# Kernel optimization log

Measured on AMD Instinct MI355X. Metric: run time of the kernel, lower is better.

The kernel has to match this reference:

```python
import jax, jax.numpy as jnp
import numpy as np

B, S, D = 2, 2048, 4096
NH, NKV = 32, 8
HD = D // NH          # 128
NREP = NH // NKV      # 4 (GQA groups)


def _rope(t, cos, sin):
    # t: [b, s, h, d]; cos/sin: [s, d//2]; interleaved (real, imag) pairs on last dim
    tr = t.reshape(*t.shape[:-1], -1, 2)
    a, b = tr[..., 0], tr[..., 1]
    c = cos[None, :, None, :]
    s = sin[None, :, None, :]
    out = jnp.stack([a * c - b * s, a * s + b * c], axis=-1)
    return out.reshape(t.shape)


def _repeat_kv(t, n_rep):
    # [b, s, n_kv, d] -> [b, s, n_kv*n_rep, d]
    b, s, nkv, d = t.shape
    return jnp.broadcast_to(t[:, :, :, None, :], (b, s, nkv, n_rep, d)).reshape(b, s, nkv * n_rep, d)


def setup_inputs() -> dict:
    key = jax.random.key(0)
    ks = jax.random.split(key, 5)
    x = jax.random.normal(ks[0], (B, S, D), jnp.float32)
    wq = jax.random.normal(ks[1], (D, NH * HD), jnp.float32) * 0.02
    wk = jax.random.normal(ks[2], (D, NKV * HD), jnp.float32) * 0.02
    wv = jax.random.normal(ks[3], (D, NKV * HD), jnp.float32) * 0.02
    wo = jax.random.normal(ks[4], (NH * HD, D), jnp.float32) * 0.02
    inv_freq = 1.0 / (10000.0 ** (jnp.arange(0, HD, 2, dtype=jnp.float32) / HD))
    angles = jnp.arange(S, dtype=jnp.float32)[:, None] * inv_freq[None, :]  # [S, HD//2]
    return {
        "x": x, "wq": wq, "wk": wk, "wv": wv, "wo": wo,
        "freqs_cos": jnp.cos(angles), "freqs_sin": jnp.sin(angles),
        "start_pos": 0,
    }


def reference(x, wq, wk, wv, wo, freqs_cos, freqs_sin, start_pos):
    b, s, _ = x.shape
    xq = (x @ wq).reshape(b, s, NH, HD)
    xk = (x @ wk).reshape(b, s, NKV, HD)
    xv = (x @ wv).reshape(b, s, NKV, HD)
    xq = _rope(xq, freqs_cos, freqs_sin)
    xk = _rope(xk, freqs_cos, freqs_sin)
    # prefill (start_pos=0): cache[:b, :s] = xk/xv, then keys/values read back equal xk/xv
    keys = _repeat_kv(xk, NREP)    # [b, s, NH, HD]
    values = _repeat_kv(xv, NREP)  # [b, s, NH, HD]
    scores = jnp.einsum("bqhd,bkhd->bhqk", xq, keys) / jnp.sqrt(jnp.float32(HD))
    probs = jax.nn.softmax(scores, axis=-1)
    out = jnp.einsum("bhqk,bkhd->bqhd", probs, values).reshape(b, s, NH * HD)
    return out @ wo
```

## Files before the change

### kernel.cpp

```cpp
#include <hip/hip_runtime.h>
#include <hip/hip_bf16.h>
#include <cstdint>

#define B_   2
#define S_   2048
#define D_   4096
#define NH_  32
#define NKV_ 8
#define HD_  128
#define BS_  (B_*S_)
#define NQK_ 6144

typedef __bf16 bf16_t;
typedef __bf16 bf16x8 __attribute__((ext_vector_type(8)));
typedef __bf16 bf16x4 __attribute__((ext_vector_type(4)));
typedef __bf16 bf16x2 __attribute__((ext_vector_type(2)));
typedef float  f32x4  __attribute__((ext_vector_type(4)));

typedef const __attribute__((address_space(1))) void* gas_ptr;
typedef __attribute__((address_space(3))) void* las_ptr;

__device__ __forceinline__ void gload_lds16(const void* g, void* l) {
  __builtin_amdgcn_global_load_lds((gas_ptr)g, (las_ptr)l, 16, 0, 0);
}

__device__ __forceinline__ float exp2_fast(float x) {
  float r;
  asm("v_exp_f32 %0, %1" : "=v"(r) : "v"(x));
  return r;
}

#define LD8(p) (*(const bf16x8*)(p))
#define MFMA(a, b, c) __builtin_amdgcn_mfma_f32_16x16x32_bf16(a, b, c, 0, 0, 0)

__global__ __launch_bounds__(256) void k_cvt(const float4* __restrict__ in,
                                             bf16x4* __restrict__ out, int n4) {
  int i = blockIdx.x * 256 + threadIdx.x;
  if (i >= n4) return;
  float4 v = in[i];
  bf16x4 o = { (bf16_t)v.x, (bf16_t)v.y, (bf16_t)v.z, (bf16_t)v.w };
  out[i] = o;
}

__global__ __launch_bounds__(256) void k_transpose_cvt(const float* __restrict__ w,
                                                       bf16_t* __restrict__ wt,
                                                       int K, int N) {
  __shared__ float tile[32][33];
  int n0 = blockIdx.x * 32, k0 = blockIdx.y * 32;
  int tx = threadIdx.x, ty = threadIdx.y;
#pragma unroll
  for (int i = 0; i < 4; i++)
    tile[ty + 8*i][tx] = w[(size_t)(k0 + ty + 8*i) * N + n0 + tx];
  __syncthreads();
#pragma unroll
  for (int i = 0; i < 4; i++)
    wt[(size_t)(n0 + ty + 8*i) * K + k0 + tx] = (bf16_t)tile[tx][ty + 8*i];
}

template <typename CT, int NF>
__global__ __launch_bounds__(512, 2) void k_gemm8p(const bf16_t* __restrict__ A,
                                                   const bf16_t* __restrict__ Bt,
                                                   CT* __restrict__ C,
                                                   int M, int N, int K) {
  __shared__ __align__(16) bf16_t As[2][256 * 64];
  __shared__ __align__(16) bf16_t Bs[2][NF * 64 * 64];
  const int tid = threadIdx.x;
  const int l = tid & 63, w = tid >> 6;
  const int lr = l & 15, lg = l >> 4;
  const int wm = w >> 2, wn = w & 3;

  const int bm = blockIdx.x, bn = blockIdx.y;

  const bf16_t* Ab = A  + (size_t)bm * 256 * K;
  const bf16_t* Bb = Bt + (size_t)bn * (NF * 64) * K;

  int st_row[4], st_col[4], st_dst[4];
#pragma unroll
  for (int j = 0; j < 4; j++) {
    int o = (j * 512 + tid) * 16;
    int row = o >> 7, cb = o & 127;
    st_row[j] = row;
    st_col[j] = (cb ^ ((row & 7) << 4)) >> 1;
    st_dst[j] = o >> 1;
  }

  int aoff[8], boff[NF];
#pragma unroll
  for (int m = 0; m < 8; m++) {
    int r = wm * 128 + m * 16 + lr;
    aoff[m] = r * 64 + (((lg * 16) ^ ((r & 7) << 4)) >> 1);
  }
#pragma unroll
  for (int n = 0; n < NF; n++) {
    int r = wn * (16 * NF) + n * 16 + lr;
    boff[n] = r * 64 + (((lg * 16) ^ ((r & 7) << 4)) >> 1);
  }

  f32x4 acc[8][NF];
#pragma unroll
  for (int m = 0; m < 8; m++)
#pragma unroll
    for (int n = 0; n < NF; n++) acc[m][n] = f32x4{0.f, 0.f, 0.f, 0.f};

  auto stageA = [&](int k, int h) {
    const int kt = k << 6;
    const int rof = h << 7;
#pragma unroll
    for (int j = 0; j < 2; j++)
      gload_lds16(Ab + (size_t)(st_row[j] + rof) * K + kt + st_col[j],
                  &As[k & 1][0] + (rof << 6) + st_dst[j]);
  };
  auto stageB = [&](int k) {
    const int kt = k << 6;
#pragma unroll
    for (int j = 0; j < NF; j++)
      gload_lds16(Bb + (size_t)st_row[j] * K + kt + st_col[j],
                  &Bs[k & 1][0] + st_dst[j]);
  };

  const int NT = K >> 6;
  stageA(0, 0); stageA(0, 1); stageB(0); stageB(1);
  if constexpr (NF == 3) asm volatile("s_waitcnt vmcnt(3)" ::: "memory");
  else                   asm volatile("s_waitcnt vmcnt(4)" ::: "memory");
  __builtin_amdgcn_s_barrier();

  for (int k = 0; k < NT; ++k) {
    const bf16_t* Ap = &As[k & 1][0];
    const bf16_t* Bp = &Bs[k & 1][0];
    const bool s1 = (k + 1 < NT), s2 = (k + 2 < NT);
    bf16x8 bfr[NF], a[4];

#pragma unroll
    for (int n = 0; n < NF; n++) bfr[n] = LD8(Bp + boff[n]);
#pragma unroll
    for (int m = 0; m < 4; m++) a[m] = LD8(Ap + aoff[m]);
    if (s1) stageA(k + 1, 0);
    __builtin_amdgcn_s_barrier();
    asm volatile("s_waitcnt lgkmcnt(0)" ::: "memory");
    __builtin_amdgcn_s_setprio(1);
#pragma unroll
    for (int m = 0; m < 4; m++)
#pragma unroll
      for (int n = 0; n < NF; n++)
        acc[m][n] = MFMA(a[m], bfr[n], acc[m][n]);
    __builtin_amdgcn_s_setprio(0);
    __builtin_amdgcn_s_barrier();

#pragma unroll
    for (int m = 0; m < 4; m++) a[m] = LD8(Ap + aoff[m + 4]);
    if (s1) stageA(k + 1, 1);
    __builtin_amdgcn_s_barrier();
    asm volatile("s_waitcnt lgkmcnt(0)" ::: "memory");
    __builtin_amdgcn_s_setprio(1);
#pragma unroll
    for (int m = 0; m < 4; m++)
#pragma unroll
      for (int n = 0; n < NF; n++)
        acc[m + 4][n] = MFMA(a[m], bfr[n], acc[m + 4][n]);
    __builtin_amdgcn_s_setprio(0);
    __builtin_amdgcn_s_barrier();

#pragma unroll
    for (int n = 0; n < NF; n++) bfr[n] = LD8(Bp + (boff[n] ^ 32));
#pragma unroll
    for (int m = 0; m < 4; m++) a[m] = LD8(Ap + (aoff[m] ^ 32));
    __builtin_amdgcn_s_barrier();
    asm volatile("s_waitcnt lgkmcnt(0)" ::: "memory");
    __builtin_amdgcn_s_setprio(1);
#pragma unroll
    for (int m = 0; m < 4; m++)
#pragma unroll
      for (int n = 0; n < NF; n++)
        acc[m][n] = MFMA(a[m], bfr[n], acc[m][n]);
    __builtin_amdgcn_s_setprio(0);
    __builtin_amdgcn_s_barrier();

#pragma unroll
    for (int m = 0; m < 4; m++) a[m] = LD8(Ap + (aoff[m + 4] ^ 32));
    if (s2) {
      stageB(k + 2);
      if constexpr (NF == 3) asm volatile("s_waitcnt vmcnt(3)" ::: "memory");
      else                   asm volatile("s_waitcnt vmcnt(4)" ::: "memory");
    } else if (s1) {
      asm volatile("s_waitcnt vmcnt(0)" ::: "memory");
    }
    __builtin_amdgcn_s_barrier();
    asm volatile("s_waitcnt lgkmcnt(0)" ::: "memory");
    __builtin_amdgcn_s_setprio(1);
#pragma unroll
    for (int m = 0; m < 4; m++)
#pragma unroll
      for (int n = 0; n < NF; n++)
        acc[m + 4][n] = MFMA(a[m], bfr[n], acc[m + 4][n]);
    __builtin_amdgcn_s_setprio(0);
    __builtin_amdgcn_s_barrier();
  }

#pragma unroll
  for (int m = 0; m < 8; m++) {
    int row0 = bm * 256 + wm * 128 + m * 16 + lg * 4;
#pragma unroll
    for (int n = 0; n < NF; n++) {
      int col = bn * (NF * 64) + wn * (16 * NF) + n * 16 + lr;
#pragma unroll
      for (int i = 0; i < 4; i++)
        C[(size_t)(row0 + i) * N + col] = (CT)acc[m][n][i];
    }
  }
}

__global__ __launch_bounds__(256) void k_rope(const bf16_t* __restrict__ qkv,
                                              const float* __restrict__ fcos,
                                              const float* __restrict__ fsin,
                                              bf16_t* __restrict__ dst,
                                              int nheads, int col_off, float mul) {
  int idx = blockIdx.x * 256 + threadIdx.x;
  int p = idx & 63;
  int h = (idx >> 6) % nheads;
  int bs = idx / (64 * nheads);
  int s = bs & (S_ - 1);
  int b = bs >> 11;
  const bf16_t* src = qkv + (size_t)bs * NQK_ + col_off + h * HD_ + 2 * p;
  bf16x2 ab = *(const bf16x2*)src;
  float a = (float)ab[0], bb = (float)ab[1];
  float c = fcos[s * 64 + p], sn = fsin[s * 64 + p];
  bf16x2 o = { (bf16_t)((a * c - bb * sn) * mul), (bf16_t)((a * sn + bb * c) * mul) };
  *(bf16x2*)(dst + ((((size_t)b * nheads + h) * S_ + s) * HD_) + 2 * p) = o;
}

__global__ __launch_bounds__(256) void k_vtrans(const bf16_t* __restrict__ qkv,
                                                bf16_t* __restrict__ vtr) {
  __shared__ bf16_t tile[32][33];
  int s0 = blockIdx.x * 32, d0 = blockIdx.y * 32, z = blockIdx.z;
  int b = z >> 3, kvh = z & 7;
  int tx = threadIdx.x, ty = threadIdx.y;
#pragma unroll
  for (int i = 0; i < 4; i++)
    tile[ty + 8*i][tx] =
        qkv[(size_t)(b * S_ + s0 + ty + 8*i) * NQK_ + (D_ + NKV_ * HD_) + kvh * HD_ + d0 + tx];
  __syncthreads();
#pragma unroll
  for (int i = 0; i < 4; i++)
    vtr[((size_t)z * HD_ + d0 + ty + 8*i) * S_ + s0 + tx] = tile[tx][ty + 8*i];
}

#define KVBLK 64
#define SM_THR 12.0f
__global__ __launch_bounds__(256, 2) void k_flash(const bf16_t* __restrict__ qr,
                                                  const bf16_t* __restrict__ kr,
                                                  const bf16_t* __restrict__ vt,
                                                  bf16_t* __restrict__ ctx) {
  __shared__ __align__(16) bf16_t Ks[2][KVBLK * HD_];
  __shared__ __align__(16) bf16_t Vs[2][HD_ * KVBLK];
  __shared__ __align__(16) char  plds[4][2048];
  const int tid = threadIdx.x;
  const int l = tid & 63, w = tid >> 6;
  const int lr = l & 15, lg = l >> 4;
  const int qb = blockIdx.x, h = blockIdx.y, b = blockIdx.z;
  const int kvh = h >> 2;

  const bf16_t* qbase = qr + (((size_t)b * NH_ + h) * S_ + qb * 128 + w * 32) * HD_;
  const bf16_t* kbase = kr + (((size_t)b * NKV_ + kvh) * S_) * HD_;
  const bf16_t* vbase = vt + (((size_t)b * NKV_ + kvh) * HD_) * S_;

  bf16x8 qf[2][4];
#pragma unroll
  for (int m = 0; m < 2; m++)
#pragma unroll
    for (int kk = 0; kk < 4; kk++)
      qf[m][kk] = *(const bf16x8*)(qbase + (m * 16 + lr) * HD_ + kk * 32 + lg * 8);

  bf16x8 ones;
#pragma unroll
  for (int j = 0; j < 8; j++) ones[j] = (bf16_t)1.0f;

  f32x4 o[2][9];
#pragma unroll
  for (int m = 0; m < 2; m++)
#pragma unroll
    for (int n = 0; n < 9; n++) o[m][n] = f32x4{0.f, 0.f, 0.f, 0.f};
  float mR[2][4];
#pragma unroll
  for (int m = 0; m < 2; m++)
#pragma unroll
    for (int i = 0; i < 4; i++) mR[m][i] = -1e30f;

  auto stage = [&](int bu, int t) {
    const int kb = t * KVBLK;
#pragma unroll
    for (int j = 0; j < 4; j++) {
      int o_ = (tid + 256 * j) * 16;
      int row = o_ >> 8, cb = o_ & 255;
      int scb = cb ^ ((row & 7) << 4);
      gload_lds16(kbase + (size_t)(kb + row) * HD_ + (scb >> 1),
                  &Ks[bu][0] + (o_ >> 1));
    }
#pragma unroll
    for (int j = 0; j < 4; j++) {
      int o_ = (tid + 256 * j) * 16;
      int row = o_ >> 7, cb = o_ & 127;
      int scb = cb ^ ((row & 7) << 4);
      gload_lds16(vbase + (size_t)row * S_ + kb + (scb >> 1),
                  &Vs[bu][0] + (o_ >> 1));
    }
  };

  const int nt = S_ / KVBLK;
  stage(0, 0);
  __syncthreads();
  int buf = 0;

  for (int t = 0; t < nt; t++) {
    if (t + 1 < nt) stage(buf ^ 1, t + 1);
    const bf16_t* Kb = &Ks[buf][0];
    const bf16_t* Vb = &Vs[buf][0];

    f32x4 sc[2][4];
#pragma unroll
    for (int m = 0; m < 2; m++)
#pragma unroll
      for (int n = 0; n < 4; n++) sc[m][n] = f32x4{0.f, 0.f, 0.f, 0.f};
    __builtin_amdgcn_s_setprio(1);
#pragma unroll
    for (int n = 0; n < 4; n++) {
#pragma unroll
      for (int kk = 0; kk < 4; kk++) {
        int r = n * 16 + lr;
        int cb = (kk * 64 + lg * 16) ^ ((r & 7) << 4);
        bf16x8 kf = *(const bf16x8*)(Kb + (((r << 8) + cb) >> 1));
        sc[0][n] = MFMA(qf[0][kk], kf, sc[0][n]);
        sc[1][n] = MFMA(qf[1][kk], kf, sc[1][n]);
      }
    }
    __builtin_amdgcn_s_setprio(0);

    bf16x8 pf[2][2];
#pragma unroll
    for (int m = 0; m < 2; m++) {
      float chk = -1e30f;
#pragma unroll
      for (int i = 0; i < 4; i++) {
        float lm = fmaxf(fmaxf(sc[m][0][i], sc[m][1][i]),
                         fmaxf(sc[m][2][i], sc[m][3][i]));
        chk = fmaxf(chk, lm - mR[m][i]);
      }
      if (!__all(chk <= SM_THR)) {
#pragma unroll
        for (int i = 0; i < 4; i++) {
          float tmx = fmaxf(fmaxf(sc[m][0][i], sc[m][1][i]),
                            fmaxf(sc[m][2][i], sc[m][3][i]));
          tmx = fmaxf(tmx, __shfl_xor(tmx, 1));
          tmx = fmaxf(tmx, __shfl_xor(tmx, 2));
          tmx = fmaxf(tmx, __shfl_xor(tmx, 4));
          tmx = fmaxf(tmx, __shfl_xor(tmx, 8));
          float mnew = fmaxf(mR[m][i], tmx);
          float alpha = exp2_fast(mR[m][i] - mnew);
          mR[m][i] = mnew;
#pragma unroll
          for (int n = 0; n < 9; n++) o[m][n][i] *= alpha;
        }
      }
#pragma unroll
      for (int n = 0; n < 4; n++)
#pragma unroll
        for (int i = 0; i < 4; i++) {
          float pv = exp2_fast(sc[m][n][i] - mR[m][i]);
          int r = lg * 4 + i;
          int cbyte = (n * 32 + lr * 2) ^ ((r & 7) << 4);
          *(bf16_t*)(&plds[w][r * 128 + cbyte]) = (bf16_t)pv;
        }
      pf[m][0] = *(const bf16x8*)(&plds[w][lr * 128 + ((lg * 16) ^ ((lr & 7) << 4))]);
      pf[m][1] = *(const bf16x8*)(&plds[w][lr * 128 + ((64 + lg * 16) ^ ((lr & 7) << 4))]);
    }

    __builtin_amdgcn_s_setprio(1);
#pragma unroll
    for (int n = 0; n < 8; n++) {
#pragma unroll
      for (int kk = 0; kk < 2; kk++) {
        int r = n * 16 + lr;
        int cb = (kk * 64 + lg * 16) ^ ((r & 7) << 4);
        bf16x8 vf = *(const bf16x8*)(Vb + (((r << 7) + cb) >> 1));
        o[0][n] = MFMA(pf[0][kk], vf, o[0][n]);
        o[1][n] = MFMA(pf[1][kk], vf, o[1][n]);
      }
    }
    o[0][8] = MFMA(pf[0][0], ones, o[0][8]);
    o[0][8] = MFMA(pf[0][1], ones, o[0][8]);
    o[1][8] = MFMA(pf[1][0], ones, o[1][8]);
    o[1][8] = MFMA(pf[1][1], ones, o[1][8]);
    __builtin_amdgcn_s_setprio(0);
    __syncthreads();
    buf ^= 1;
  }

#pragma unroll
  for (int m = 0; m < 2; m++)
#pragma unroll
    for (int i = 0; i < 4; i++) {
      float inv = 1.0f / o[m][8][i];
      int srow = qb * 128 + w * 32 + m * 16 + lg * 4 + i;
#pragma unroll
      for (int n = 0; n < 8; n++) {
        int d = n * 16 + lr;
        ctx[((size_t)(b * S_ + srow)) * D_ + h * HD_ + d] = (bf16_t)(o[m][n][i] * inv);
      }
    }
}

extern "C" void kernel_launch(void* const* d_in, const int* in_sizes, int n_in,
                              void* d_out, int out_size, void* d_ws, size_t ws_size,
                              hipStream_t stream) {
  const float* x    = (const float*)d_in[0];
  const float* wq   = (const float*)d_in[1];
  const float* wk   = (const float*)d_in[2];
  const float* wv   = (const float*)d_in[3];
  const float* wo   = (const float*)d_in[4];
  const float* fcos = (const float*)d_in[5];
  const float* fsin = (const float*)d_in[6];
  float* out = (float*)d_out;

  const size_t SZ_XB    = (size_t)BS_ * D_ * 2;
  const size_t SZ_WQKVT = (size_t)NQK_ * D_ * 2;
  const size_t SZ_WOT   = (size_t)D_ * D_ * 2;
  char* p = (char*)d_ws;
  bf16_t* xb    = (bf16_t*)p;
  bf16_t* wqkvt = (bf16_t*)(p + SZ_XB);
  bf16_t* wot   = (bf16_t*)(p + SZ_XB + SZ_WQKVT);
  bf16_t* qkv   = (bf16_t*)(p + SZ_XB + SZ_WQKVT + SZ_WOT);
  bf16_t* qrope = xb;
  bf16_t* krope = wqkvt;
  bf16_t* vtr   = wqkvt + (size_t)BS_ * NKV_ * HD_;
  bf16_t* ctx   = qkv;

  const float QSCALE = (float)(0.08838834764831845 * 1.4426950408889634);

  dim3 tb(32, 8);
  k_cvt<<<BS_ * D_ / 1024, 256, 0, stream>>>((const float4*)x, (bf16x4*)xb, BS_ * D_ / 4);
  k_transpose_cvt<<<dim3(D_ / 32, D_ / 32), tb, 0, stream>>>(wq, wqkvt, D_, D_);
  k_transpose_cvt<<<dim3(32, D_ / 32), tb, 0, stream>>>(wk, wqkvt + (size_t)D_ * D_, D_, NKV_ * HD_);
  k_transpose_cvt<<<dim3(32, D_ / 32), tb, 0, stream>>>(wv, wqkvt + (size_t)(D_ + NKV_ * HD_) * D_, D_, NKV_ * HD_);
  k_transpose_cvt<<<dim3(D_ / 32, D_ / 32), tb, 0, stream>>>(wo, wot, D_, D_);
  k_gemm8p<bf16_t, 3><<<dim3(BS_ / 256, NQK_ / 192), 512, 0, stream>>>(xb, wqkvt, qkv, BS_, NQK_, D_);
  k_rope<<<BS_ * NH_ * 64 / 256, 256, 0, stream>>>(qkv, fcos, fsin, qrope, NH_, 0, QSCALE);
  k_rope<<<BS_ * NKV_ * 64 / 256, 256, 0, stream>>>(qkv, fcos, fsin, krope, NKV_, D_, 1.0f);
  k_vtrans<<<dim3(S_ / 32, HD_ / 32, B_ * NKV_), tb, 0, stream>>>(qkv, vtr);
  k_flash<<<dim3(S_ / 128, NH_, B_), 256, 0, stream>>>(qrope, krope, vtr, ctx);
  k_gemm8p<float, 4><<<dim3(BS_ / 256, D_ / 256), 512, 0, stream>>>(ctx, wot, out, BS_, D_, D_);
}
```

Measured before the change: 606.7 us.

## Transpose QK^T MFMA operands and shuffle P through registers instead of LDS

Swaps the A/B operands of the score MFMA so each lane holds one query row's scores. The row max then comes from an in-lane reduction plus two cross-lane shuffles, and each lane keeps a single running max per row. The P tile is now packed with v_cvt_pk_bf16 and rearranged into the PV operand layout with ds_bpermute, replacing the per-element LDS stores and reloads and their scratch buffer. This removes LDS traffic and shuffle work from the softmax step but adds bpermute operations and a per-row alpha broadcast. The remaining 60 lines of the kernel, which finalize with mR, are not shown and may need matching changes.

```diff
diff --git a/kernel.cpp b/kernel.cpp
--- a/kernel.cpp
+++ b/kernel.cpp
@@ -16,6 +16,7 @@
 typedef __bf16 bf16x4 __attribute__((ext_vector_type(4)));
 typedef __bf16 bf16x2 __attribute__((ext_vector_type(2)));
 typedef float  f32x4  __attribute__((ext_vector_type(4)));
+typedef unsigned uint32x4 __attribute__((ext_vector_type(4)));
 
 typedef const __attribute__((address_space(1))) void* gas_ptr;
 typedef __attribute__((address_space(3))) void* las_ptr;
@@ -27,6 +28,12 @@
 __device__ __forceinline__ float exp2_fast(float x) {
   float r;
   asm("v_exp_f32 %0, %1" : "=v"(r) : "v"(x));
+  return r;
+}
+
+__device__ __forceinline__ unsigned cvt_pk_bf16(float a, float b) {
+  unsigned r;
+  asm("v_cvt_pk_bf16_f32 %0, %1, %2" : "=v"(r) : "v"(a), "v"(b));
   return r;
 }
 
@@ -252,7 +259,6 @@
                                                   bf16_t* __restrict__ ctx) {
   __shared__ __align__(16) bf16_t Ks[2][KVBLK * HD_];
   __shared__ __align__(16) bf16_t Vs[2][HD_ * KVBLK];
-  __shared__ __align__(16) char  plds[4][2048];
   const int tid = threadIdx.x;
   const int l = tid & 63, w = tid >> 6;
   const int lr = l & 15, lg = l >> 4;
@@ -263,6 +269,9 @@
   const bf16_t* kbase = kr + (((size_t)b * NKV_ + kvh) * S_) * HD_;
   const bf16_t* vbase = vt + (((size_t)b * NKV_ + kvh) * HD_) * S_;
 
+  const int sl0 = (lr + ((lg & 1) << 5)) << 2;
+  const int sl1 = sl0 + (16 << 2);
+
   bf16x8 qf[2][4];
 #pragma unroll
   for (int m = 0; m < 2; m++)
@@ -279,11 +288,7 @@
   for (int m = 0; m < 2; m++)
 #pragma unroll
     for (int n = 0; n < 9; n++) o[m][n] = f32x4{0.f, 0.f, 0.f, 0.f};
-  float mR[2][4];
-#pragma unroll
-  for (int m = 0; m < 2; m++)
-#pragma unroll
-    for (int i = 0; i < 4; i++) mR[m][i] = -1e30f;
+  float mR[2] = {-1e30f, -1e30f};
 
   auto stage = [&](int bu, int t) {
     const int kb = t * KVBLK;
@@ -328,8 +333,8 @@
         int r = n * 16 + lr;
         int cb = (kk * 64 + lg * 16) ^ ((r & 7) << 4);
         bf16x8 kf = *(const bf16x8*)(Kb + (((r << 8) + cb) >> 1));
-        sc[0][n] = MFMA(qf[0][kk], kf, sc[0][n]);
-        sc[1][n] = MFMA(qf[1][kk], kf, sc[1][n]);
+        sc[0][n] = MFMA(kf, qf[0][kk], sc[0][n]);
+        sc[1][n] = MFMA(kf, qf[1][kk], sc[1][n]);
       }
     }
     __builtin_amdgcn_s_setprio(0);
@@ -337,40 +342,48 @@
     bf16x8 pf[2][2];
 #pragma unroll
     for (int m = 0; m < 2; m++) {
-      float chk = -1e30f;
-#pragma unroll
-      for (int i = 0; i < 4; i++) {
-        float lm = fmaxf(fmaxf(sc[m][0][i], sc[m][1][i]),
-                         fmaxf(sc[m][2][i], sc[m][3][i]));
-        chk = fmaxf(chk, lm - mR[m][i]);
-      }
-      if (!__all(chk <= SM_THR)) {
-#pragma unroll
-        for (int i = 0; i < 4; i++) {
-          float tmx = fmaxf(fmaxf(sc[m][0][i], sc[m][1][i]),
-                            fmaxf(sc[m][2][i], sc[m][3][i]));
-          tmx = fmaxf(tmx, __shfl_xor(tmx, 1));
-          tmx = fmaxf(tmx, __shfl_xor(tmx, 2));
-          tmx = fmaxf(tmx, __shfl_xor(tmx, 4));
-          tmx = fmaxf(tmx, __shfl_xor(tmx, 8));
-          float mnew = fmaxf(mR[m][i], tmx);
-          float alpha = exp2_fast(mR[m][i] - mnew);
-          mR[m][i] = mnew;
-#pragma unroll
-          for (int n = 0; n < 9; n++) o[m][n][i] *= alpha;
+      float lm = sc[m][0][0];
+#pragma unroll
+      for (int n = 0; n < 4; n++)
+#pragma unroll
+        for (int i = 0; i < 4; i++)
+          if (n | i) lm = fmaxf(lm, sc[m][n][i]);
+      if (!__all(lm - mR[m] <= SM_THR)) {
+        float tmx = fmaxf(lm, __shfl_xor(lm, 16));
+        tmx = fmaxf(tmx, __shfl_xor(tmx, 32));
+        float mnew = fmaxf(mR[m], tmx);
+        float alpha = exp2_fast(mR[m] - mnew);
+        mR[m] = mnew;
+        float av[4];
+#pragma unroll
+        for (int i = 0; i < 4; i++) av[i] = __shfl(alpha, lg * 4 + i);
+#pragma unroll
+        for (int n = 0; n < 9; n++)
+#pragma unroll
+          for (int i = 0; i < 4; i++) o[m][n][i] *= av[i];
+      }
+      unsigned W[4][2];
+#pragma unroll
+      for (int n = 0; n < 4; n++) {
+        float p0 = exp2_fast(sc[m][n][0] - mR[m]);
+        float p1 = exp2_fast(sc[m][n][1] - mR[m]);
+        float p2 = exp2_fast(sc[m][n][2] - mR[m]);
+        float p3 = exp2_fast(sc[m][n][3] - mR[m]);
+        W[n][0] = cvt_pk_bf16(p0, p1);
+        W[n][1] = cvt_pk_bf16(p2, p3);
+      }
+#pragma unroll
+      for (int kk = 0; kk < 2; kk++) {
+        uint32x4 wv;
+#pragma unroll
+        for (int t = 0; t < 4; t++) {
+          int srcb = (t < 2) ? sl0 : sl1;
+          unsigned lo = (unsigned)__builtin_amdgcn_ds_bpermute(srcb, (int)W[2 * kk][t & 1]);
+          unsigned hi = (unsigned)__builtin_amdgcn_ds_bpermute(srcb, (int)W[2 * kk + 1][t & 1]);
+          wv[t] = (l & 32) ? hi : lo;
         }
-      }
-#pragma unroll
-      for (int n = 0; n < 4; n++)
-#pragma unroll
-        for (int i = 0; i < 4; i++) {
-          float pv = exp2_fast(sc[m][n][i] - mR[m][i]);
-          int r = lg * 4 + i;
-          int cbyte = (n * 32 + lr * 2) ^ ((r & 7) << 4);
-          *(bf16_t*)(&plds[w][r * 128 + cbyte]) = (bf16_t)pv;
-        }
-      pf[m][0] = *(const bf16x8*)(&plds[w][lr * 128 + ((lg * 16) ^ ((lr & 7) << 4))]);
-      pf[m][1] = *(const bf16x8*)(&plds[w][lr * 128 + ((64 + lg * 16) ^ ((lr & 7) << 4))]);
+        pf[m][kk] = __builtin_bit_cast(bf16x8, wv);
+      }
     }
 
     __builtin_amdgcn_s_setprio(1);
```

New measurement: 606.0 us. Within noise of the previous version (-0.1%).
